# Performance work log

Measured on AMD Instinct MI355X. Metric: run time of the kernel, lower is better.

## Reference

```python
import jax, jax.numpy as jnp
import numpy as np

B, N, NREL = 8, 512, 4096
IN_DIM, REL_DIM = 64, 32
NF_PART, NF_REL, NF_EFF, OUT_DIM = 128, 256, 128, 64


def _lin(key, fan_in, fan_out):
    kw, kb = jax.random.split(key)
    s = 1.0 / np.sqrt(fan_in)
    w = jax.random.uniform(kw, (fan_in, fan_out), jnp.float32, -s, s)
    b = jax.random.uniform(kb, (fan_out,), jnp.float32, -s, s)
    return w, b


def setup_inputs() -> dict:
    key = jax.random.key(0)
    ks = jax.random.split(key, 16)
    state = jax.random.normal(ks[0], (B, N, IN_DIM), jnp.float32)
    # one-hot receiver / sender incidence matrices [B, N, NREL]
    recv = jax.random.randint(ks[1], (B, NREL), 0, N)
    send = jax.random.randint(ks[2], (B, NREL), 0, N)
    Rr = jnp.transpose(jax.nn.one_hot(recv, N, dtype=jnp.float32), (0, 2, 1))
    Rs = jnp.transpose(jax.nn.one_hot(send, N, dtype=jnp.float32), (0, 2, 1))
    Ra = jax.random.normal(ks[3], (B, NREL, REL_DIM), jnp.float32)

    pe0_w, pe0_b = _lin(ks[4], IN_DIM, NF_PART)
    pe1_w, pe1_b = _lin(ks[5], NF_PART, NF_PART)
    pe2_w, pe2_b = _lin(ks[6], NF_PART, NF_EFF)
    re_in = 2 * IN_DIM + REL_DIM
    re0_w, re0_b = _lin(ks[7], re_in, NF_REL)
    re1_w, re1_b = _lin(ks[8], NF_REL, NF_REL)
    re2_w, re2_b = _lin(ks[9], NF_REL, NF_REL)
    rp_w, rp_b = _lin(ks[10], NF_REL + 2 * NF_EFF, NF_EFF)   # relation propagator
    pp_w, pp_b = _lin(ks[11], 2 * NF_EFF, NF_EFF)            # particle propagator
    pr0_w, pr0_b = _lin(ks[12], NF_EFF, NF_EFF)
    pr1_w, pr1_b = _lin(ks[13], NF_EFF, OUT_DIM)

    return dict(state=state, Rr=Rr, Rs=Rs, Ra=Ra,
                pe0_w=pe0_w, pe0_b=pe0_b, pe1_w=pe1_w, pe1_b=pe1_b,
                pe2_w=pe2_w, pe2_b=pe2_b,
                re0_w=re0_w, re0_b=re0_b, re1_w=re1_w, re1_b=re1_b,
                re2_w=re2_w, re2_b=re2_b,
                rp_w=rp_w, rp_b=rp_b, pp_w=pp_w, pp_b=pp_b,
                pr0_w=pr0_w, pr0_b=pr0_b, pr1_w=pr1_w, pr1_b=pr1_b,
                pstep=3)


def _mlp3(x, w0, b0, w1, b1, w2, b2):
    x = jax.nn.relu(x @ w0 + b0)
    x = jax.nn.relu(x @ w1 + b1)
    return jax.nn.relu(x @ w2 + b2)


def reference(state, Rr, Rs, Ra,
              pe0_w, pe0_b, pe1_w, pe1_b, pe2_w, pe2_b,
              re0_w, re0_b, re1_w, re1_b, re2_w, re2_b,
              rp_w, rp_b, pp_w, pp_b,
              pr0_w, pr0_b, pr1_w, pr1_b, pstep):
    Rrp = jnp.transpose(Rr, (0, 2, 1))  # [B, NREL, N]
    Rsp = jnp.transpose(Rs, (0, 2, 1))
    state_r = Rrp @ state               # [B, NREL, IN_DIM]
    state_s = Rsp @ state

    particle_encode = _mlp3(state, pe0_w, pe0_b, pe1_w, pe1_b, pe2_w, pe2_b)
    relation_encode = _mlp3(jnp.concatenate([state_r, state_s, Ra], axis=2),
                            re0_w, re0_b, re1_w, re1_b, re2_w, re2_b)

    particle_effect = jnp.zeros((state.shape[0], state.shape[1], NF_EFF),
                                dtype=state.dtype)
    for _ in range(pstep):
        effect_r = Rrp @ particle_effect           # gather to relations
        effect_s = Rsp @ particle_effect
        relation_effect = jax.nn.relu(
            jnp.concatenate([relation_encode, effect_r, effect_s], axis=2)
            @ rp_w + rp_b)
        effect_agg = Rr @ relation_effect          # scatter to particles
        particle_effect = jax.nn.relu(
            jnp.concatenate([particle_encode, effect_agg], axis=2)
            @ pp_w + pp_b)

    h = jax.nn.relu(particle_effect @ pr0_w + pr0_b)
    return h @ pr1_w + pr1_b                       # [B, N, OUT_DIM]
```

## Files before the change

### kernel.cpp

```cpp
#include <hip/hip_runtime.h>
#include <hip/hip_bf16.h>

#define BC    8
#define NC    512
#define NRELC 4096
#define MAXDEG 64

typedef unsigned short u16;
typedef __attribute__((ext_vector_type(2))) float  f32x2;
typedef __attribute__((ext_vector_type(4))) float  f32x4;
typedef __attribute__((ext_vector_type(8))) __bf16 bf16x8;
typedef __attribute__((ext_vector_type(8))) short  s16x8;
typedef __attribute__((ext_vector_type(2))) u16    u16x2;
typedef __attribute__((ext_vector_type(4))) u16    u16x4;
typedef __attribute__((ext_vector_type(4))) int    i32x4;

__device__ __forceinline__ u16 f2b(float f) {
  union { float f; unsigned u; } v; v.f = f;
  unsigned u = v.u;
  return (u16)((u + 0x7fffu + ((u >> 16) & 1u)) >> 16);
}

template<int KBLK>
__device__ __forceinline__ int toff(int row, int k) {
  return (row >> 4) * (KBLK * 256) + ((k >> 3) << 8) + ((row & 15) << 4) + ((k & 7) << 1);
}

__global__ __launch_bounds__(256) void onehot_matvec(
    const float* __restrict__ Rr, const float* __restrict__ Rs,
    int* __restrict__ recv, int* __restrict__ send) {
  int blk = blockIdx.x;
  int tens = blk >> 8;
  int b = (blk >> 5) & 7;
  int rt = blk & 31;
  const float* srcf = (tens ? Rs : Rr) + (long)b * NC * NRELC + rt * 128;
  int* dst = (tens ? send : recv) + b * NRELC + rt * 128;
  int ng = threadIdx.x >> 5;
  int col = threadIdx.x & 31;
  const f32x4* cp = (const f32x4*)srcf + col;
  f32x4 acc = (f32x4){0.f, 0.f, 0.f, 0.f};
#pragma unroll 8
  for (int i = 0; i < 64; ++i) {
    int n = ng * 64 + i;
    f32x4 x = cp[(long)n * (NRELC / 4)];
    float w = (float)n;
    acc[0] = fmaf(x[0], w, acc[0]);
    acc[1] = fmaf(x[1], w, acc[1]);
    acc[2] = fmaf(x[2], w, acc[2]);
    acc[3] = fmaf(x[3], w, acc[3]);
  }
  __shared__ f32x4 red[256];
  red[threadIdx.x] = acc;
  __syncthreads();
  if (threadIdx.x < 32) {
    f32x4 s = red[threadIdx.x];
#pragma unroll
    for (int g = 1; g < 8; ++g) {
      f32x4 t = red[g * 32 + threadIdx.x];
      s[0] += t[0]; s[1] += t[1]; s[2] += t[2]; s[3] += t[3];
    }
    i32x4 o;
    o[0] = (int)s[0]; o[1] = (int)s[1]; o[2] = (int)s[2]; o[3] = (int)s[3];
    *(i32x4*)&dst[threadIdx.x * 4] = o;
  }
}

struct WT13 {
  const float* src[13];
  u16* dst[13];
  int K[13], N[13];
  int cum[14];
};

__global__ void wtrans_v2(WT13 wt) {
  int idx = blockIdx.x * 256 + threadIdx.x;
  if (idx >= wt.cum[13]) return;
  int w = 0;
  while (idx >= wt.cum[w + 1]) ++w;
  int j = idx - wt.cum[w];
  int N = wt.N[w], K = wt.K[w];
  int k = j / N, n = j - k * N;
  wt.dst[w][n * K + k] = f2b(wt.src[w][j]);
}

template<int MT, int NT, bool AF32>
__device__ __forceinline__ void tile_gemm(const void* __restrict__ Ap, long rowBase,
                                          const u16* __restrict__ Wt, int n0,
                                          int K, int rl, int kg, f32x4 acc[MT][NT]) {
#pragma unroll
  for (int mt = 0; mt < MT; ++mt)
#pragma unroll
    for (int t = 0; t < NT; ++t) acc[mt][t] = (f32x4){0.f, 0.f, 0.f, 0.f};

  for (int k0 = 0; k0 < K; k0 += 32) {
    int kk = k0 + kg * 8;
    bf16x8 af[MT];
#pragma unroll
    for (int mt = 0; mt < MT; ++mt) {
      long row = rowBase + mt * 16 + rl;
      if (AF32) {
        const float* ap = (const float*)Ap + row * K + kk;
        f32x4 lo = *(const f32x4*)ap;
        f32x4 hi = *(const f32x4*)(ap + 4);
        s16x8 s;
        s[0] = (short)f2b(lo[0]); s[1] = (short)f2b(lo[1]);
        s[2] = (short)f2b(lo[2]); s[3] = (short)f2b(lo[3]);
        s[4] = (short)f2b(hi[0]); s[5] = (short)f2b(hi[1]);
        s[6] = (short)f2b(hi[2]); s[7] = (short)f2b(hi[3]);
        af[mt] = __builtin_bit_cast(bf16x8, s);
      } else {
        af[mt] = *reinterpret_cast<const bf16x8*>((const u16*)Ap + row * K + kk);
      }
    }
#pragma unroll
    for (int t = 0; t < NT; ++t) {
      bf16x8 bf = *reinterpret_cast<const bf16x8*>(Wt + (size_t)(n0 + t * 16 + rl) * K + kk);
#pragma unroll
      for (int mt = 0; mt < MT; ++mt)
        acc[mt][t] = __builtin_amdgcn_mfma_f32_16x16x32_bf16(af[mt], bf, acc[mt][t], 0, 0, 0);
    }
  }
}

template<int MT, int NT, bool OBF16, bool RELU>
__device__ __forceinline__ void tile_store(void* Cp, const float* bias, const float* addC,
                                           long rowBase, int n0, int NLD,
                                           int rl, int kg, f32x4 acc[MT][NT]) {
#pragma unroll
  for (int mt = 0; mt < MT; ++mt) {
    long orow = rowBase + mt * 16 + kg * 4;
#pragma unroll
    for (int t = 0; t < NT; ++t) {
      int gc = n0 + t * 16 + rl;
      float bv = bias ? bias[gc] : 0.f;
#pragma unroll
      for (int r = 0; r < 4; ++r) {
        long gr = orow + r;
        float v = acc[mt][t][r] + bv;
        if (addC) v += addC[gr * NLD + gc];
        if (RELU) v = fmaxf(v, 0.f);
        if (OBF16) ((u16*)Cp)[gr * NLD + gc] = f2b(v);
        else       ((float*)Cp)[gr * NLD + gc] = v;
      }
    }
  }
}

template<int KD, int NTt>
__device__ __forceinline__ void lds_layer_v4(const char* bufIn, const u16* __restrict__ Wt,
                                             int n0, int rl, int kg, f32x4 acc[4][NTt]) {
  constexpr int KI = KD / 32;
  bf16x8 bw[NTt][KI];
#pragma unroll
  for (int t = 0; t < NTt; ++t)
#pragma unroll
    for (int ki = 0; ki < KI; ++ki)
      bw[t][ki] = *(const bf16x8*)(Wt + (size_t)(n0 + t * 16 + rl) * KD + ki * 32 + kg * 8);
#pragma unroll
  for (int mt = 0; mt < 4; ++mt)
#pragma unroll
    for (int t = 0; t < NTt; ++t) acc[mt][t] = (f32x4){0.f, 0.f, 0.f, 0.f};
#pragma unroll
  for (int ki = 0; ki < KI; ++ki) {
    int kk = ki * 32 + kg * 8;
    bf16x8 af[4];
#pragma unroll
    for (int mt = 0; mt < 4; ++mt)
      af[mt] = *(const bf16x8*)&bufIn[toff<32>(mt * 16 + rl, kk)];
#pragma unroll
    for (int t = 0; t < NTt; ++t)
#pragma unroll
      for (int mt = 0; mt < 4; ++mt)
        acc[mt][t] = __builtin_amdgcn_mfma_f32_16x16x32_bf16(af[mt], bw[t][ki], acc[mt][t], 0, 0, 0);
  }
}

template<int NTt>
__device__ __forceinline__ void lds_store_v4(char* bufOut, const float* __restrict__ bias,
                                             int n0, int rl, int kg, f32x4 acc[4][NTt]) {
#pragma unroll
  for (int mt = 0; mt < 4; ++mt)
#pragma unroll
    for (int t = 0; t < NTt; ++t) {
      int gc = n0 + t * 16 + rl;
      float bv = bias[gc];
#pragma unroll
      for (int r = 0; r < 4; ++r) {
        int row = mt * 16 + kg * 4 + r;
        *(u16*)&bufOut[toff<32>(row, gc)] = f2b(fmaxf(acc[mt][t][r] + bv, 0.f));
      }
    }
}

__global__ __launch_bounds__(512, 3) void k2_kernel(
    const int* __restrict__ recv, const int* __restrict__ send,
    int* __restrict__ deg, int* __restrict__ lists,
    const float* __restrict__ state, const float* __restrict__ Ra,
    const u16* __restrict__ re0t, const float* __restrict__ re0_b,
    const u16* __restrict__ re1t, const float* __restrict__ re1_b,
    const u16* __restrict__ re2t, const float* __restrict__ re2_b,
    const u16* __restrict__ rp0t, const float* __restrict__ rp_b,
    float* __restrict__ rbase,
    const u16* __restrict__ pe0t, const float* __restrict__ pe0_b,
    const u16* __restrict__ pe1t, const float* __restrict__ pe1_b,
    const u16* __restrict__ pe2t, const float* __restrict__ pe2_b,
    const u16* __restrict__ pp0t, const float* __restrict__ pp_b,
    u16* __restrict__ x1, u16* __restrict__ x2, u16* __restrict__ penc,
    float* __restrict__ pbase) {
  __shared__ char bufA[32768];
  __shared__ char bufB[32768];
  int tid = threadIdx.x;
  int wid = tid >> 6, lane = tid & 63;
  int blk = blockIdx.x;

  if (blk >= 1024) {
    int rl = lane & 15, kg = lane >> 4;
    long rowBase = (blk - 1024) * 16;
    f32x4 acc[1][1];
    tile_gemm<1, 1, true>(state, rowBase, pe0t, wid * 16, 64, rl, kg, acc);
    tile_store<1, 1, true, true>(x1, pe0_b, nullptr, rowBase, wid * 16, 128, rl, kg, acc);
    __syncthreads();
    tile_gemm<1, 1, false>(x1, rowBase, pe1t, wid * 16, 128, rl, kg, acc);
    tile_store<1, 1, true, true>(x2, pe1_b, nullptr, rowBase, wid * 16, 128, rl, kg, acc);
    __syncthreads();
    tile_gemm<1, 1, false>(x2, rowBase, pe2t, wid * 16, 128, rl, kg, acc);
    tile_store<1, 1, true, true>(penc, pe2_b, nullptr, rowBase, wid * 16, 128, rl, kg, acc);
    __syncthreads();
    tile_gemm<1, 1, false>(penc, rowBase, pp0t, wid * 16, 128, rl, kg, acc);
    tile_store<1, 1, false, false>(pbase, pp_b, nullptr, rowBase, wid * 16, 128, rl, kg, acc);
    return;
  }
  if (blk >= 512) {
    int bn = (blk - 512) * 8 + wid;
    int b = bn >> 9, n = bn & 511;
    const int* rv = recv + (long)b * NRELC;
    int base = 0;
    for (int c = 0; c < 64; ++c) {
      int r = c * 64 + lane;
      bool ok = (rv[r] == n);
      unsigned long long m = __ballot(ok);
      if (ok) {
        int rank = __popcll(m & ((1ull << lane) - 1ull));
        lists[(long)bn * MAXDEG + base + rank] = r;
      }
      base += (int)__popcll(m);
    }
    if (lane == 0) deg[bn] = base;
    return;
  }

  int m0 = blk * 64;
  for (int c = tid; c < 64 * 40; c += 512) {
    int row = c / 40;
    int c4 = (c - row * 40) * 4;
    int grow = m0 + row;
    int b = grow >> 12;
    f32x4 v;
    if (c4 < 64)       v = *(const f32x4*)&state[((long)(b * NC + recv[grow])) * 64 + c4];
    else if (c4 < 128) v = *(const f32x4*)&state[((long)(b * NC + send[grow])) * 64 + (c4 - 64)];
    else               v = *(const f32x4*)&Ra[(long)grow * 32 + (c4 - 128)];
    u16x4 o;
    o[0] = f2b(v[0]); o[1] = f2b(v[1]); o[2] = f2b(v[2]); o[3] = f2b(v[3]);
    *(u16x4*)&bufA[toff<32>(row, c4)] = o;
  }
  __syncthreads();

  int rl = lane & 15, kg = lane >> 4;
  f32x4 acc[4][2];
  lds_layer_v4<160, 2>(bufA, re0t, wid * 32, rl, kg, acc);
  lds_store_v4<2>(bufB, re0_b, wid * 32, rl, kg, acc);
  __syncthreads();
  lds_layer_v4<256, 2>(bufB, re1t, wid * 32, rl, kg, acc);
  lds_store_v4<2>(bufA, re1_b, wid * 32, rl, kg, acc);
  __syncthreads();
  lds_layer_v4<256, 2>(bufA, re2t, wid * 32, rl, kg, acc);
  lds_store_v4<2>(bufB, re2_b, wid * 32, rl, kg, acc);
  __syncthreads();
  f32x4 acc2[4][1];
  lds_layer_v4<256, 1>(bufB, rp0t, wid * 16, rl, kg, acc2);
#pragma unroll
  for (int mt = 0; mt < 4; ++mt) {
    int gc = wid * 16 + rl;
    float bv = rp_b[gc];
#pragma unroll
    for (int r = 0; r < 4; ++r) {
      long gr = m0 + mt * 16 + kg * 4 + r;
      rbase[gr * 128 + gc] = acc2[mt][0][r] + bv;
    }
  }
}

__global__ __launch_bounds__(512, 4) void relstep_v4(
    const u16* __restrict__ peff, const u16* __restrict__ rp1t,
    const u16* __restrict__ rp2t, const float* __restrict__ rbase,
    const int* __restrict__ recv, const int* __restrict__ send,
    float* __restrict__ tmp) {
  __shared__ char ebuf0[16384];
  __shared__ char ebuf1[16384];
  int tid = threadIdx.x;
  int m0 = blockIdx.x * 64;

  for (int c = tid; c < 2048; c += 512) {
    int s = c >> 10, rem = c & 1023, row = rem >> 4, ch = rem & 15;
    int gr = m0 + row;
    int b = gr >> 12;
    int idx = s ? send[gr] : recv[gr];
    bf16x8 v = *(const bf16x8*)&peff[((long)(b * NC + idx)) * 128 + ch * 8];
    char* dst = s ? ebuf1 : ebuf0;
    *(bf16x8*)&dst[toff<16>(row, ch * 8)] = v;
  }
  __syncthreads();

  int wid = tid >> 6, lane = tid & 63;
  int rl = lane & 15, kg = lane >> 4;
  int wm = wid >> 2, wn = wid & 3;
  int n0 = wn * 32;

  bf16x8 b1[2][4], b2[2][4];
#pragma unroll
  for (int t = 0; t < 2; ++t)
#pragma unroll
    for (int ki = 0; ki < 4; ++ki) {
      b1[t][ki] = *(const bf16x8*)(rp1t + (size_t)(n0 + t * 16 + rl) * 128 + ki * 32 + kg * 8);
      b2[t][ki] = *(const bf16x8*)(rp2t + (size_t)(n0 + t * 16 + rl) * 128 + ki * 32 + kg * 8);
    }

  f32x4 acc[2][2];
#pragma unroll
  for (int mt = 0; mt < 2; ++mt)
#pragma unroll
    for (int t = 0; t < 2; ++t) acc[mt][t] = (f32x4){0.f, 0.f, 0.f, 0.f};

#pragma unroll
  for (int ki = 0; ki < 4; ++ki) {
    int kk = ki * 32 + kg * 8;
    bf16x8 e0[2], e1[2];
#pragma unroll
    for (int mt = 0; mt < 2; ++mt) {
      int row = wm * 32 + mt * 16 + rl;
      e0[mt] = *(const bf16x8*)&ebuf0[toff<16>(row, kk)];
      e1[mt] = *(const bf16x8*)&ebuf1[toff<16>(row, kk)];
    }
#pragma unroll
    for (int t = 0; t < 2; ++t)
#pragma unroll
      for (int mt = 0; mt < 2; ++mt)
        acc[mt][t] = __builtin_amdgcn_mfma_f32_16x16x32_bf16(e0[mt], b1[t][ki], acc[mt][t], 0, 0, 0);
#pragma unroll
    for (int t = 0; t < 2; ++t)
#pragma unroll
      for (int mt = 0; mt < 2; ++mt)
        acc[mt][t] = __builtin_amdgcn_mfma_f32_16x16x32_bf16(e1[mt], b2[t][ki], acc[mt][t], 0, 0, 0);
  }

#pragma unroll
  for (int mt = 0; mt < 2; ++mt) {
#pragma unroll
    for (int r = 0; r < 4; ++r) {
      long gr = m0 + wm * 32 + mt * 16 + kg * 4 + r;
      const float* rb = &rbase[gr * 128];
      float* dst = &tmp[gr * 128];
#pragma unroll
      for (int t = 0; t < 2; ++t) {
        int gc = n0 + t * 16 + rl;
        dst[gc] = fmaxf(acc[mt][t][r] + rb[gc], 0.f);
      }
    }
  }
}

template<bool RELU>
__global__ __launch_bounds__(256) void segreduce_kernel(
    const float* __restrict__ src, const int* __restrict__ deg,
    const int* __restrict__ lists, u16* __restrict__ agg16) {
  int wid = threadIdx.x >> 6, lane = threadIdx.x & 63;
  int p = blockIdx.x * 4 + wid;
  int b = p >> 9;
  int c = lane * 2;
  int d = deg[p];
  const int* lp = &lists[(long)p * MAXDEG];
  f32x2 acc = (f32x2){0.f, 0.f};
  for (int k = 0; k < d; ++k) {
    long row = ((long)b * NRELC + lp[k]) * 128;
    f32x2 v = *(const f32x2*)&src[row + c];
    if (RELU) { v[0] = fmaxf(v[0], 0.f); v[1] = fmaxf(v[1], 0.f); }
    acc[0] += v[0]; acc[1] += v[1];
  }
  u16x2 o;
  o[0] = f2b(acc[0]); o[1] = f2b(acc[1]);
  *(u16x2*)&agg16[(long)p * 128 + c] = o;
}

__global__ __launch_bounds__(256) void ppgemm_v2(
    const u16* __restrict__ agg16, const u16* __restrict__ pp1t,
    const float* __restrict__ pbase, u16* __restrict__ peff) {
  int wid = threadIdx.x >> 6, lane = threadIdx.x & 63;
  int rl = lane & 15, kg = lane >> 4;
  long rowBase = blockIdx.x * 16;
  f32x4 acc[1][2];
  tile_gemm<1, 2, false>(agg16, rowBase, pp1t, wid * 32, 128, rl, kg, acc);
  tile_store<1, 2, true, true>(peff, nullptr, pbase, rowBase, wid * 32, 128, rl, kg, acc);
}

__global__ __launch_bounds__(256) void ppdec_kernel(
    const u16* __restrict__ agg16, const u16* __restrict__ pp1t,
    const float* __restrict__ pbase,
    const u16* __restrict__ pr0t, const float* __restrict__ pr0_b,
    const u16* __restrict__ pr1t, const float* __restrict__ pr1_b,
    float* __restrict__ out) {
  __shared__ char t0[4096];
  __shared__ char t1[4096];
  int wid = threadIdx.x >> 6, lane = threadIdx.x & 63;
  int rl = lane & 15, kg = lane >> 4;
  long rowBase = blockIdx.x * 16;

  f32x4 acc[1][2];
  tile_gemm<1, 2, false>(agg16, rowBase, pp1t, wid * 32, 128, rl, kg, acc);
#pragma unroll
  for (int t = 0; t < 2; ++t) {
    int gc = wid * 32 + t * 16 + rl;
#pragma unroll
    for (int r = 0; r < 4; ++r) {
      int row = kg * 4 + r;
      float v = acc[0][t][r] + pbase[(rowBase + row) * 128 + gc];
      *(u16*)&t0[toff<16>(row, gc)] = f2b(fmaxf(v, 0.f));
    }
  }
  __syncthreads();

  f32x4 a2[2];
  a2[0] = (f32x4){0.f, 0.f, 0.f, 0.f};
  a2[1] = (f32x4){0.f, 0.f, 0.f, 0.f};
#pragma unroll
  for (int ki = 0; ki < 4; ++ki) {
    int kk = ki * 32 + kg * 8;
    bf16x8 af = *(const bf16x8*)&t0[toff<16>(rl, kk)];
#pragma unroll
    for (int t = 0; t < 2; ++t) {
      bf16x8 bf = *(const bf16x8*)(pr0t + (size_t)(wid * 32 + t * 16 + rl) * 128 + kk);
      a2[t] = __builtin_amdgcn_mfma_f32_16x16x32_bf16(af, bf, a2[t], 0, 0, 0);
    }
  }
#pragma unroll
  for (int t = 0; t < 2; ++t) {
    int gc = wid * 32 + t * 16 + rl;
    float bv = pr0_b[gc];
#pragma unroll
    for (int r = 0; r < 4; ++r) {
      int row = kg * 4 + r;
      *(u16*)&t1[toff<16>(row, gc)] = f2b(fmaxf(a2[t][r] + bv, 0.f));
    }
  }
  __syncthreads();

  if (wid < 4) {
    f32x4 a3 = (f32x4){0.f, 0.f, 0.f, 0.f};
#pragma unroll
    for (int ki = 0; ki < 4; ++ki) {
      int kk = ki * 32 + kg * 8;
      bf16x8 af = *(const bf16x8*)&t1[toff<16>(rl, kk)];
      bf16x8 bf = *(const bf16x8*)(pr1t + (size_t)(wid * 16 + rl) * 128 + kk);
      a3 = __builtin_amdgcn_mfma_f32_16x16x32_bf16(af, bf, a3, 0, 0, 0);
    }
    int gc = wid * 16 + rl;
    float bv = pr1_b[gc];
#pragma unroll
    for (int r = 0; r < 4; ++r) {
      long gr = rowBase + kg * 4 + r;
      out[gr * 64 + gc] = a3[r] + bv;
    }
  }
}

extern "C" void kernel_launch(void* const* d_in, const int* in_sizes, int n_in,
                              void* d_out, int out_size, void* d_ws, size_t ws_size,
                              hipStream_t stream) {
  const float* state = (const float*)d_in[0];
  const float* Rr    = (const float*)d_in[1];
  const float* Rs    = (const float*)d_in[2];
  const float* Ra    = (const float*)d_in[3];
  const float* pe0_w = (const float*)d_in[4];  const float* pe0_b = (const float*)d_in[5];
  const float* pe1_w = (const float*)d_in[6];  const float* pe1_b = (const float*)d_in[7];
  const float* pe2_w = (const float*)d_in[8];  const float* pe2_b = (const float*)d_in[9];
  const float* re0_w = (const float*)d_in[10]; const float* re0_b = (const float*)d_in[11];
  const float* re1_w = (const float*)d_in[12]; const float* re1_b = (const float*)d_in[13];
  const float* re2_w = (const float*)d_in[14]; const float* re2_b = (const float*)d_in[15];
  const float* rp_w  = (const float*)d_in[16]; const float* rp_b  = (const float*)d_in[17];
  const float* pp_w  = (const float*)d_in[18]; const float* pp_b  = (const float*)d_in[19];
  const float* pr0_w = (const float*)d_in[20]; const float* pr0_b = (const float*)d_in[21];
  const float* pr1_w = (const float*)d_in[22]; const float* pr1_b = (const float*)d_in[23];

  char* base = (char*)d_ws; size_t off = 0;
  auto alloc = [&](size_t b) -> void* {
    void* p = base + off; off = (off + b + 255) & ~(size_t)255; return p;
  };

  int* recv  = (int*)alloc(4L * BC * NRELC);
  int* send  = (int*)alloc(4L * BC * NRELC);
  int* deg   = (int*)alloc(4L * BC * NC);
  int* lists = (int*)alloc(4L * BC * NC * MAXDEG);
  u16* pe0t = (u16*)alloc(2L * 128 * 64);
  u16* pe1t = (u16*)alloc(2L * 128 * 128);
  u16* pe2t = (u16*)alloc(2L * 128 * 128);
  u16* re0t = (u16*)alloc(2L * 256 * 160);
  u16* re1t = (u16*)alloc(2L * 256 * 256);
  u16* re2t = (u16*)alloc(2L * 256 * 256);
  u16* rp0t = (u16*)alloc(2L * 128 * 256);
  u16* rp1t = (u16*)alloc(2L * 128 * 128);
  u16* rp2t = (u16*)alloc(2L * 128 * 128);
  u16* pp0t = (u16*)alloc(2L * 128 * 128);
  u16* pp1t = (u16*)alloc(2L * 128 * 128);
  u16* pr0t = (u16*)alloc(2L * 128 * 128);
  u16* pr1t = (u16*)alloc(2L * 64 * 128);
  float* tmp   = (float*)alloc(4L * 32768 * 128);
  float* rbase = (float*)alloc(4L * 32768 * 128);
  u16* x1   = (u16*)alloc(2L * 4096 * 128);
  u16* x2   = (u16*)alloc(2L * 4096 * 128);
  u16* penc = (u16*)alloc(2L * 4096 * 128);
  float* pbase = (float*)alloc(4L * 4096 * 128);
  u16* agg16 = (u16*)alloc(2L * 4096 * 128);
  u16* peff = (u16*)alloc(2L * 4096 * 128);
  (void)ws_size; (void)in_sizes; (void)n_in; (void)out_size;

  struct WSpec { const float* src; u16* dst; int K, N; };
  const WSpec specs[13] = {
      {pe0_w,            pe0t, 64, 128},
      {pe1_w,            pe1t, 128, 128},
      {pe2_w,            pe2t, 128, 128},
      {re0_w,            re0t, 160, 256},
      {re1_w,            re1t, 256, 256},
      {re2_w,            re2t, 256, 256},
      {rp_w,             rp0t, 256, 128},
      {rp_w + 256 * 128, rp1t, 128, 128},
      {rp_w + 384 * 128, rp2t, 128, 128},
      {pp_w,             pp0t, 128, 128},
      {pp_w + 128 * 128, pp1t, 128, 128},
      {pr0_w,            pr0t, 128, 128},
      {pr1_w,            pr1t, 128, 64},
  };
  WT13 wt;
  int cum = 0;
  for (int i = 0; i < 13; ++i) {
    wt.src[i] = specs[i].src; wt.dst[i] = specs[i].dst;
    wt.K[i] = specs[i].K; wt.N[i] = specs[i].N;
    wt.cum[i] = cum; cum += specs[i].K * specs[i].N;
  }
  wt.cum[13] = cum;

  onehot_matvec<<<512, 256, 0, stream>>>(Rr, Rs, recv, send);
  wtrans_v2<<<(cum + 255) / 256, 256, 0, stream>>>(wt);

  k2_kernel<<<1280, 512, 0, stream>>>(recv, send, deg, lists, state, Ra,
                                      re0t, re0_b, re1t, re1_b, re2t, re2_b,
                                      rp0t, rp_b, rbase,
                                      pe0t, pe0_b, pe1t, pe1_b, pe2t, pe2_b,
                                      pp0t, pp_b, x1, x2, penc, pbase);

  segreduce_kernel<true><<<1024, 256, 0, stream>>>(rbase, deg, lists, agg16);
  ppgemm_v2<<<256, 256, 0, stream>>>(agg16, pp1t, pbase, peff);
  for (int s = 1; s < 3; ++s) {
    relstep_v4<<<512, 512, 0, stream>>>(peff, rp1t, rp2t, rbase, recv, send, tmp);
    segreduce_kernel<false><<<1024, 256, 0, stream>>>(tmp, deg, lists, agg16);
    if (s == 2) break;
    ppgemm_v2<<<256, 256, 0, stream>>>(agg16, pp1t, pbase, peff);
  }

  ppdec_kernel<<<256, 256, 0, stream>>>(agg16, pp1t, pbase,
                                        pr0t, pr0_b, pr1t, pr1_b, (float*)d_out);
}
```

Baseline: 167.8 us.

## Split fused mega-kernel into CSR/particle-encoder and relation-encoder kernels, chain particle MLP through LDS

```diff
diff --git a/kernel.cpp b/kernel.cpp
--- a/kernel.cpp
+++ b/kernel.cpp
@@ -122,116 +122,19 @@
   }
 }
 
-template<int MT, int NT, bool OBF16, bool RELU>
-__device__ __forceinline__ void tile_store(void* Cp, const float* bias, const float* addC,
-                                           long rowBase, int n0, int NLD,
-                                           int rl, int kg, f32x4 acc[MT][NT]) {
-#pragma unroll
-  for (int mt = 0; mt < MT; ++mt) {
-    long orow = rowBase + mt * 16 + kg * 4;
-#pragma unroll
-    for (int t = 0; t < NT; ++t) {
-      int gc = n0 + t * 16 + rl;
-      float bv = bias ? bias[gc] : 0.f;
-#pragma unroll
-      for (int r = 0; r < 4; ++r) {
-        long gr = orow + r;
-        float v = acc[mt][t][r] + bv;
-        if (addC) v += addC[gr * NLD + gc];
-        if (RELU) v = fmaxf(v, 0.f);
-        if (OBF16) ((u16*)Cp)[gr * NLD + gc] = f2b(v);
-        else       ((float*)Cp)[gr * NLD + gc] = v;
-      }
-    }
-  }
-}
-
-template<int KD, int NTt>
-__device__ __forceinline__ void lds_layer_v4(const char* bufIn, const u16* __restrict__ Wt,
-                                             int n0, int rl, int kg, f32x4 acc[4][NTt]) {
-  constexpr int KI = KD / 32;
-  bf16x8 bw[NTt][KI];
-#pragma unroll
-  for (int t = 0; t < NTt; ++t)
-#pragma unroll
-    for (int ki = 0; ki < KI; ++ki)
-      bw[t][ki] = *(const bf16x8*)(Wt + (size_t)(n0 + t * 16 + rl) * KD + ki * 32 + kg * 8);
-#pragma unroll
-  for (int mt = 0; mt < 4; ++mt)
-#pragma unroll
-    for (int t = 0; t < NTt; ++t) acc[mt][t] = (f32x4){0.f, 0.f, 0.f, 0.f};
-#pragma unroll
-  for (int ki = 0; ki < KI; ++ki) {
-    int kk = ki * 32 + kg * 8;
-    bf16x8 af[4];
-#pragma unroll
-    for (int mt = 0; mt < 4; ++mt)
-      af[mt] = *(const bf16x8*)&bufIn[toff<32>(mt * 16 + rl, kk)];
-#pragma unroll
-    for (int t = 0; t < NTt; ++t)
-#pragma unroll
-      for (int mt = 0; mt < 4; ++mt)
-        acc[mt][t] = __builtin_amdgcn_mfma_f32_16x16x32_bf16(af[mt], bw[t][ki], acc[mt][t], 0, 0, 0);
-  }
-}
-
-template<int NTt>
-__device__ __forceinline__ void lds_store_v4(char* bufOut, const float* __restrict__ bias,
-                                             int n0, int rl, int kg, f32x4 acc[4][NTt]) {
-#pragma unroll
-  for (int mt = 0; mt < 4; ++mt)
-#pragma unroll
-    for (int t = 0; t < NTt; ++t) {
-      int gc = n0 + t * 16 + rl;
-      float bv = bias[gc];
-#pragma unroll
-      for (int r = 0; r < 4; ++r) {
-        int row = mt * 16 + kg * 4 + r;
-        *(u16*)&bufOut[toff<32>(row, gc)] = f2b(fmaxf(acc[mt][t][r] + bv, 0.f));
-      }
-    }
-}
-
-__global__ __launch_bounds__(512, 3) void k2_kernel(
-    const int* __restrict__ recv, const int* __restrict__ send,
-    int* __restrict__ deg, int* __restrict__ lists,
-    const float* __restrict__ state, const float* __restrict__ Ra,
-    const u16* __restrict__ re0t, const float* __restrict__ re0_b,
-    const u16* __restrict__ re1t, const float* __restrict__ re1_b,
-    const u16* __restrict__ re2t, const float* __restrict__ re2_b,
-    const u16* __restrict__ rp0t, const float* __restrict__ rp_b,
-    float* __restrict__ rbase,
+__global__ __launch_bounds__(256) void csr_partenc_v2(
+    const int* __restrict__ recv, int* __restrict__ deg, int* __restrict__ lists,
+    const float* __restrict__ state,
     const u16* __restrict__ pe0t, const float* __restrict__ pe0_b,
     const u16* __restrict__ pe1t, const float* __restrict__ pe1_b,
     const u16* __restrict__ pe2t, const float* __restrict__ pe2_b,
     const u16* __restrict__ pp0t, const float* __restrict__ pp_b,
-    u16* __restrict__ x1, u16* __restrict__ x2, u16* __restrict__ penc,
     float* __restrict__ pbase) {
-  __shared__ char bufA[32768];
-  __shared__ char bufB[32768];
-  int tid = threadIdx.x;
-  int wid = tid >> 6, lane = tid & 63;
-  int blk = blockIdx.x;
-
-  if (blk >= 1024) {
-    int rl = lane & 15, kg = lane >> 4;
-    long rowBase = (blk - 1024) * 16;
-    f32x4 acc[1][1];
-    tile_gemm<1, 1, true>(state, rowBase, pe0t, wid * 16, 64, rl, kg, acc);
-    tile_store<1, 1, true, true>(x1, pe0_b, nullptr, rowBase, wid * 16, 128, rl, kg, acc);
-    __syncthreads();
-    tile_gemm<1, 1, false>(x1, rowBase, pe1t, wid * 16, 128, rl, kg, acc);
-    tile_store<1, 1, true, true>(x2, pe1_b, nullptr, rowBase, wid * 16, 128, rl, kg, acc);
-    __syncthreads();
-    tile_gemm<1, 1, false>(x2, rowBase, pe2t, wid * 16, 128, rl, kg, acc);
-    tile_store<1, 1, true, true>(penc, pe2_b, nullptr, rowBase, wid * 16, 128, rl, kg, acc);
-    __syncthreads();
-    tile_gemm<1, 1, false>(penc, rowBase, pp0t, wid * 16, 128, rl, kg, acc);
-    tile_store<1, 1, false, false>(pbase, pp_b, nullptr, rowBase, wid * 16, 128, rl, kg, acc);
-    return;
-  }
-  if (blk >= 512) {
-    int bn = (blk - 512) * 8 + wid;
+  __shared__ char t0[4096];
+  __shared__ char t1[4096];
+  int wid = threadIdx.x >> 6, lane = threadIdx.x & 63;
+  if (blockIdx.x < 1024) {
+    int bn = blockIdx.x * 4 + wid;
     int b = bn >> 9, n = bn & 511;
     const int* rv = recv + (long)b * NRELC;
     int base = 0;
@@ -248,8 +151,149 @@
     if (lane == 0) deg[bn] = base;
     return;
   }
-
-  int m0 = blk * 64;
+  int rl = lane & 15, kg = lane >> 4;
+  long rowBase = (blockIdx.x - 1024) * 16;
+
+  f32x4 acc[1][2];
+  tile_gemm<1, 2, true>(state, rowBase, pe0t, wid * 32, 64, rl, kg, acc);
+#pragma unroll
+  for (int t = 0; t < 2; ++t) {
+    int gc = wid * 32 + t * 16 + rl;
+    float bv = pe0_b[gc];
+#pragma unroll
+    for (int r = 0; r < 4; ++r)
+      *(u16*)&t0[toff<16>(kg * 4 + r, gc)] = f2b(fmaxf(acc[0][t][r] + bv, 0.f));
+  }
+  __syncthreads();
+
+  f32x4 a2[2];
+  a2[0] = (f32x4){0.f, 0.f, 0.f, 0.f};
+  a2[1] = (f32x4){0.f, 0.f, 0.f, 0.f};
+#pragma unroll
+  for (int ki = 0; ki < 4; ++ki) {
+    int kk = ki * 32 + kg * 8;
+    bf16x8 af = *(const bf16x8*)&t0[toff<16>(rl, kk)];
+#pragma unroll
+    for (int t = 0; t < 2; ++t) {
+      bf16x8 bf = *(const bf16x8*)(pe1t + (size_t)(wid * 32 + t * 16 + rl) * 128 + kk);
+      a2[t] = __builtin_amdgcn_mfma_f32_16x16x32_bf16(af, bf, a2[t], 0, 0, 0);
+    }
+  }
+#pragma unroll
+  for (int t = 0; t < 2; ++t) {
+    int gc = wid * 32 + t * 16 + rl;
+    float bv = pe1_b[gc];
+#pragma unroll
+    for (int r = 0; r < 4; ++r)
+      *(u16*)&t1[toff<16>(kg * 4 + r, gc)] = f2b(fmaxf(a2[t][r] + bv, 0.f));
+  }
+  __syncthreads();
+
+  a2[0] = (f32x4){0.f, 0.f, 0.f, 0.f};
+  a2[1] = (f32x4){0.f, 0.f, 0.f, 0.f};
+#pragma unroll
+  for (int ki = 0; ki < 4; ++ki) {
+    int kk = ki * 32 + kg * 8;
+    bf16x8 af = *(const bf16x8*)&t1[toff<16>(rl, kk)];
+#pragma unroll
+    for (int t = 0; t < 2; ++t) {
+      bf16x8 bf = *(const bf16x8*)(pe2t + (size_t)(wid * 32 + t * 16 + rl) * 128 + kk);
+      a2[t] = __builtin_amdgcn_mfma_f32_16x16x32_bf16(af, bf, a2[t], 0, 0, 0);
+    }
+  }
+#pragma unroll
+  for (int t = 0; t < 2; ++t) {
+    int gc = wid * 32 + t * 16 + rl;
+    float bv = pe2_b[gc];
+#pragma unroll
+    for (int r = 0; r < 4; ++r)
+      *(u16*)&t0[toff<16>(kg * 4 + r, gc)] = f2b(fmaxf(a2[t][r] + bv, 0.f));
+  }
+  __syncthreads();
+
+  a2[0] = (f32x4){0.f, 0.f, 0.f, 0.f};
+  a2[1] = (f32x4){0.f, 0.f, 0.f, 0.f};
+#pragma unroll
+  for (int ki = 0; ki < 4; ++ki) {
+    int kk = ki * 32 + kg * 8;
+    bf16x8 af = *(const bf16x8*)&t0[toff<16>(rl, kk)];
+#pragma unroll
+    for (int t = 0; t < 2; ++t) {
+      bf16x8 bf = *(const bf16x8*)(pp0t + (size_t)(wid * 32 + t * 16 + rl) * 128 + kk);
+      a2[t] = __builtin_amdgcn_mfma_f32_16x16x32_bf16(af, bf, a2[t], 0, 0, 0);
+    }
+  }
+#pragma unroll
+  for (int t = 0; t < 2; ++t) {
+    int gc = wid * 32 + t * 16 + rl;
+    float bv = pp_b[gc];
+#pragma unroll
+    for (int r = 0; r < 4; ++r) {
+      long gr = rowBase + kg * 4 + r;
+      pbase[gr * 128 + gc] = a2[t][r] + bv;
+    }
+  }
+}
+
+template<int KD, int NTt>
+__device__ __forceinline__ void lds_layer_v4(const char* bufIn, const u16* __restrict__ Wt,
+                                             int n0, int rl, int kg, f32x4 acc[4][NTt]) {
+  constexpr int KI = KD / 32;
+  bf16x8 bw[NTt][KI];
+#pragma unroll
+  for (int t = 0; t < NTt; ++t)
+#pragma unroll
+    for (int ki = 0; ki < KI; ++ki)
+      bw[t][ki] = *(const bf16x8*)(Wt + (size_t)(n0 + t * 16 + rl) * KD + ki * 32 + kg * 8);
+#pragma unroll
+  for (int mt = 0; mt < 4; ++mt)
+#pragma unroll
+    for (int t = 0; t < NTt; ++t) acc[mt][t] = (f32x4){0.f, 0.f, 0.f, 0.f};
+#pragma unroll
+  for (int ki = 0; ki < KI; ++ki) {
+    int kk = ki * 32 + kg * 8;
+    bf16x8 af[4];
+#pragma unroll
+    for (int mt = 0; mt < 4; ++mt)
+      af[mt] = *(const bf16x8*)&bufIn[toff<32>(mt * 16 + rl, kk)];
+#pragma unroll
+    for (int t = 0; t < NTt; ++t)
+#pragma unroll
+      for (int mt = 0; mt < 4; ++mt)
+        acc[mt][t] = __builtin_amdgcn_mfma_f32_16x16x32_bf16(af[mt], bw[t][ki], acc[mt][t], 0, 0, 0);
+  }
+}
+
+template<int NTt>
+__device__ __forceinline__ void lds_store_v4(char* bufOut, const float* __restrict__ bias,
+                                             int n0, int rl, int kg, f32x4 acc[4][NTt]) {
+#pragma unroll
+  for (int mt = 0; mt < 4; ++mt)
+#pragma unroll
+    for (int t = 0; t < NTt; ++t) {
+      int gc = n0 + t * 16 + rl;
+      float bv = bias[gc];
+#pragma unroll
+      for (int r = 0; r < 4; ++r) {
+        int row = mt * 16 + kg * 4 + r;
+        *(u16*)&bufOut[toff<32>(row, gc)] = f2b(fmaxf(acc[mt][t][r] + bv, 0.f));
+      }
+    }
+}
+
+__global__ __launch_bounds__(512, 3) void relenc_fused_v4(
+    const float* __restrict__ state, const float* __restrict__ Ra,
+    const int* __restrict__ recv, const int* __restrict__ send,
+    const u16* __restrict__ re0t, const float* __restrict__ re0_b,
+    const u16* __restrict__ re1t, const float* __restrict__ re1_b,
+    const u16* __restrict__ re2t, const float* __restrict__ re2_b,
+    const u16* __restrict__ rp0t, const float* __restrict__ rp_b,
+    float* __restrict__ rbase) {
+  __shared__ char bufA[32768];
+  __shared__ char bufB[32768];
+  int tid = threadIdx.x;
+  int m0 = blockIdx.x * 64;
+
   for (int c = tid; c < 64 * 40; c += 512) {
     int row = c / 40;
     int c4 = (c - row * 40) * 4;
@@ -265,7 +309,9 @@
   }
   __syncthreads();
 
+  int wid = tid >> 6, lane = tid & 63;
   int rl = lane & 15, kg = lane >> 4;
+
   f32x4 acc[4][2];
   lds_layer_v4<160, 2>(bufA, re0t, wid * 32, rl, kg, acc);
   lds_store_v4<2>(bufB, re0_b, wid * 32, rl, kg, acc);
@@ -399,7 +445,16 @@
   long rowBase = blockIdx.x * 16;
   f32x4 acc[1][2];
   tile_gemm<1, 2, false>(agg16, rowBase, pp1t, wid * 32, 128, rl, kg, acc);
-  tile_store<1, 2, true, true>(peff, nullptr, pbase, rowBase, wid * 32, 128, rl, kg, acc);
+#pragma unroll
+  for (int t = 0; t < 2; ++t) {
+    int gc = wid * 32 + t * 16 + rl;
+#pragma unroll
+    for (int r = 0; r < 4; ++r) {
+      long gr = rowBase + kg * 4 + r;
+      float v = acc[0][t][r] + pbase[gr * 128 + gc];
+      peff[gr * 128 + gc] = f2b(fmaxf(v, 0.f));
+    }
+  }
 }
 
 __global__ __launch_bounds__(256) void ppdec_kernel(
@@ -514,9 +569,6 @@
   u16* pr1t = (u16*)alloc(2L * 64 * 128);
   float* tmp   = (float*)alloc(4L * 32768 * 128);
   float* rbase = (float*)alloc(4L * 32768 * 128);
-  u16* x1   = (u16*)alloc(2L * 4096 * 128);
-  u16* x2   = (u16*)alloc(2L * 4096 * 128);
-  u16* penc = (u16*)alloc(2L * 4096 * 128);
   float* pbase = (float*)alloc(4L * 4096 * 128);
   u16* agg16 = (u16*)alloc(2L * 4096 * 128);
   u16* peff = (u16*)alloc(2L * 4096 * 128);
@@ -550,11 +602,12 @@
   onehot_matvec<<<512, 256, 0, stream>>>(Rr, Rs, recv, send);
   wtrans_v2<<<(cum + 255) / 256, 256, 0, stream>>>(wt);
 
-  k2_kernel<<<1280, 512, 0, stream>>>(recv, send, deg, lists, state, Ra,
-                                      re0t, re0_b, re1t, re1_b, re2t, re2_b,
-                                      rp0t, rp_b, rbase,
-                                      pe0t, pe0_b, pe1t, pe1_b, pe2t, pe2_b,
-                                      pp0t, pp_b, x1, x2, penc, pbase);
+  csr_partenc_v2<<<1280, 256, 0, stream>>>(recv, deg, lists, state,
+                                           pe0t, pe0_b, pe1t, pe1_b, pe2t, pe2_b,
+                                           pp0t, pp_b, pbase);
+  relenc_fused_v4<<<512, 512, 0, stream>>>(state, Ra, recv, send,
+                                           re0t, re0_b, re1t, re1_b, re2t, re2_b,
+                                           rp0t, rp_b, rbase);
 
   segreduce_kernel<true><<<1024, 256, 0, stream>>>(rbase, deg, lists, agg16);
   ppgemm_v2<<<256, 256, 0, stream>>>(agg16, pp1t, pbase, peff);
```

New measurement: 161.4 us. 1.04x faster.
